# Performance work log

Hardware: AMD Instinct MI355X
Metric: run time of the kernel (lower is better)

Reference implementation:

```python
import jax, jax.numpy as jnp
import numpy as np


def setup_inputs() -> dict:
    key = jax.random.key(0)
    k1, k2 = jax.random.split(key)
    B, N, Fin, Fout, K = 4, 4096, 64, 64, 20
    x = jax.random.normal(k1, (B, N, Fin), dtype=jnp.float32)
    # nn.Linear(2*Fin, Fout): weight [Fout, 2*Fin], bias [Fout]
    W = jax.random.normal(k2, (Fout, 2 * Fin), dtype=jnp.float32) * (1.0 / np.sqrt(2 * Fin))
    b = jnp.zeros((Fout,), dtype=jnp.float32)
    return {"x": x, "W": W, "b": b, "k": K}


def _edge_features(x, k):
    # x: [B, N, F] -> edge features [B, N, k, 2F]
    # pairwise squared distance: ||xi||^2 - 2 xi.xj + ||xj||^2
    xs = jnp.sum(x * x, axis=2, keepdims=True)            # [B, N, 1]
    dist = xs - 2.0 * jnp.einsum('bnf,bmf->bnm', x, x) + jnp.swapaxes(xs, 1, 2)  # [B, N, N]
    idx = jnp.argsort(dist, axis=2)[:, :, 1:k + 1]        # skip self -> [B, N, k]
    # gather neighbor features per batch (vectorized index_select)
    neighbors = jax.vmap(lambda xb, ib: xb[ib])(x, idx)   # [B, N, k, F]
    central = jnp.broadcast_to(x[:, :, None, :], neighbors.shape)
    return jnp.concatenate([central, neighbors - central], axis=3)  # [B, N, k, 2F]


def reference(x, W, b, k):
    ee = _edge_features(x, k)                 # [B, N, k, 2F]
    h = jnp.einsum('bnkc,oc->bnko', ee, W) + b  # Linear(2F -> Fout)
    return jnp.max(h, axis=2)                 # max over k neighbors -> [B, N, Fout]
```

## Files before the change

### kernel.cpp

```cpp
#include <hip/hip_runtime.h>
#include <float.h>


constexpr int Bb = 4, Nn = 4096, Ff = 64, Kk = 20;

typedef __attribute__((ext_vector_type(8))) short bf16x8;
typedef __attribute__((ext_vector_type(16))) float f32x16;

__device__ inline unsigned int bf16rn(float f) {
  unsigned int u = __float_as_uint(f);
  return (u + 0x7fffu + ((u >> 16) & 1u)) >> 16;
}

constexpr int RT1 = 16;

__global__ __launch_bounds__(256) void uv_kernel2(
    const float* __restrict__ x, const float* __restrict__ W,
    const float* __restrict__ bvec, float* __restrict__ u,
    float* __restrict__ v, float* __restrict__ sq,
    unsigned short* __restrict__ xhi, unsigned short* __restrict__ xlo) {
  __shared__ __align__(16) float4 Ws[64 * 33];
  __shared__ __align__(16) float4 xs[RT1 * 16];
  const int t = threadIdx.x, l = t & 63, w = t >> 6;
  const int bn0 = blockIdx.x * RT1;
  #pragma unroll
  for (int i = 0; i < 8; i++) {
    int f = t + 256 * i;
    Ws[(f >> 5) * 33 + (f & 31)] = ((const float4*)W)[f];
  }
  xs[t] = ((const float4*)x)[bn0 * 16 + t];
  __syncthreads();
  #pragma unroll
  for (int i = 0; i < 4; i++) {
    int idx = t + 256 * i;
    int nloc = idx >> 6;
    int k = idx & 63;
    float val = ((const float*)xs)[idx];
    unsigned int hb = bf16rn(val);
    float fhi = __uint_as_float(hb << 16);
    unsigned int lb = bf16rn(val - fhi);
    int ng = bn0 + nloc;
    size_t flat = ((size_t)(ng >> 5) << 11) + ((size_t)(k >> 4) << 9) +
                  ((size_t)((k >> 3) & 1) << 8) + ((size_t)(ng & 31) << 3) +
                  (size_t)(k & 7);
    xhi[flat] = (unsigned short)hb;
    xlo[flat] = (unsigned short)lb;
  }
  #pragma unroll
  for (int i = 0; i < 4; i++) {
    int r = 4 * w + i;
    float val = ((const float*)&xs[r * 16])[l];
    float s = val * val;
    #pragma unroll
    for (int d = 32; d; d >>= 1) s += __shfl_xor(s, d, 64);
    if (l == 0) sq[bn0 + r] = s;
  }
  const int o = l;
  float ua[4] = {0.f, 0.f, 0.f, 0.f}, va[4] = {0.f, 0.f, 0.f, 0.f};
  #pragma unroll
  for (int c = 0; c < 16; c++) {
    float4 w1 = Ws[o * 33 + c];
    float4 w2 = Ws[o * 33 + 16 + c];
    float4 wd;
    wd.x = w1.x - w2.x; wd.y = w1.y - w2.y;
    wd.z = w1.z - w2.z; wd.w = w1.w - w2.w;
    #pragma unroll
    for (int i = 0; i < 4; i++) {
      float4 xv = xs[(4 * w + i) * 16 + c];
      ua[i] += xv.x * wd.x + xv.y * wd.y + xv.z * wd.z + xv.w * wd.w;
      va[i] += xv.x * w2.x + xv.y * w2.y + xv.z * w2.z + xv.w * w2.w;
    }
  }
  float bo = bvec[o];
  #pragma unroll
  for (int i = 0; i < 4; i++) {
    size_t row = (size_t)(bn0 + 4 * w + i);
    u[row * 64 + o] = ua[i] + bo;
    v[row * 64 + o] = va[i];
  }
}


__global__ __launch_bounds__(256) void key_mfma_kernel(
    const unsigned short* __restrict__ xhi,
    const unsigned short* __restrict__ xlo, const float* __restrict__ sq,
    unsigned short* __restrict__ keys) {
  const int t = threadIdx.x, l = t & 63, w = t >> 6;
  const int blk = blockIdx.x;
  const int b = blk >> 9;
  const int r = blk & 511;
  const int n_base = (r >> 2) * 32;
  const int m0w = (r & 3) * 1024 + w * 256;
  const int col = l & 31, half = l >> 5;

  const unsigned short* xhb = xhi + (size_t)b * Nn * Ff;
  const unsigned short* xlb = xlo + (size_t)b * Nn * Ff;
  const float* sqb = sq + b * Nn;

  bf16x8 Ahi[4], Alo[4];
  #pragma unroll
  for (int ks = 0; ks < 4; ks++) {
    size_t off = ((size_t)((n_base >> 5) * 4 + ks) << 9) + ((size_t)l << 3);
    Ahi[ks] = *(const bf16x8*)(xhb + off);
    Alo[ks] = *(const bf16x8*)(xlb + off);
  }
  float sqn_r[16];
  #pragma unroll
  for (int e = 0; e < 16; e++) {
    int row = (e & 3) + 8 * (e >> 2) + 4 * half;
    sqn_r[e] = sqb[n_base + row];
  }

  for (int j = 0; j < 8; ++j) {
    const int m0 = m0w + 32 * j;
    const int mblk = m0 >> 5;
    bf16x8 Bhi[4], Blo[4];
    #pragma unroll
    for (int ks = 0; ks < 4; ks++) {
      size_t off = ((size_t)(mblk * 4 + ks) << 9) + ((size_t)l << 3);
      Bhi[ks] = *(const bf16x8*)(xhb + off);
      Blo[ks] = *(const bf16x8*)(xlb + off);
    }
    f32x16 acc = {0.f, 0.f, 0.f, 0.f, 0.f, 0.f, 0.f, 0.f,
                  0.f, 0.f, 0.f, 0.f, 0.f, 0.f, 0.f, 0.f};
    #pragma unroll
    for (int ks = 0; ks < 4; ks++) {
      acc = __builtin_amdgcn_mfma_f32_32x32x16_bf16(Ahi[ks], Bhi[ks], acc, 0, 0, 0);
      acc = __builtin_amdgcn_mfma_f32_32x32x16_bf16(Ahi[ks], Blo[ks], acc, 0, 0, 0);
      acc = __builtin_amdgcn_mfma_f32_32x32x16_bf16(Alo[ks], Bhi[ks], acc, 0, 0, 0);
    }
    const int m = m0 + col;
    const float sm = sqb[m];
    #pragma unroll
    for (int e = 0; e < 16; e++) {
      int row = (e & 3) + 8 * (e >> 2) + 4 * half;
      int n = n_base + row;
      float d = fmaxf(sqn_r[e] + sm - 2.0f * acc[e], 0.f);
      unsigned int key = __float_as_uint(d) >> 15;
      if (m == n) key = 0xFFFFu;
      keys[((size_t)(b * Nn + n) << 12) + m] = (unsigned short)key;
    }
  }
}

__global__ __launch_bounds__(256) void select_kernel(
    const float* __restrict__ x, const unsigned short* __restrict__ keys,
    const float* __restrict__ u, const float* __restrict__ v,
    float* __restrict__ out) {
  __shared__ int candS[4 * 64];
  __shared__ unsigned long long keyS[4 * 64];
  __shared__ unsigned int histS[4][256];
  const int t = threadIdx.x, l = t & 63, w = t >> 6;
  const int row = blockIdx.x * 4 + w;
  const int rowu = __builtin_amdgcn_readfirstlane(row);
  const int b = rowu >> 12, n = rowu & (Nn - 1);
  const uint4* kr = (const uint4*)(keys + (size_t)rowu * Nn);
  uint4 kv[8];
  #pragma unroll
  for (int j = 0; j < 8; j++) kv[j] = kr[j * 64 + l];

  #pragma unroll
  for (int i = 0; i < 4; i++) histS[w][4 * l + i] = 0u;

  auto countLE = [&](int mid) -> int {
    int c = 0;
    #pragma unroll
    for (int j = 0; j < 8; j++) {
      unsigned int a0 = kv[j].x, a1 = kv[j].y, a2 = kv[j].z, a3 = kv[j].w;
      c += ((int)(a0 & 0xffffu) <= mid) + ((int)(a0 >> 16) <= mid);
      c += ((int)(a1 & 0xffffu) <= mid) + ((int)(a1 >> 16) <= mid);
      c += ((int)(a2 & 0xffffu) <= mid) + ((int)(a2 >> 16) <= mid);
      c += ((int)(a3 & 0xffffu) <= mid) + ((int)(a3 >> 16) <= mid);
    }
    #pragma unroll
    for (int d2 = 1; d2 < 64; d2 <<= 1) c += __shfl_xor(c, d2, 64);
    return c;
  };

  unsigned int mn = 0xffffffffu;
  #pragma unroll
  for (int j = 0; j < 8; j++) {
    unsigned int a0 = kv[j].x, a1 = kv[j].y, a2 = kv[j].z, a3 = kv[j].w;
    mn = min(mn, min(min(a0 & 0xffffu, a0 >> 16), min(a1 & 0xffffu, a1 >> 16)));
    mn = min(mn, min(min(a2 & 0xffffu, a2 >> 16), min(a3 & 0xffffu, a3 >> 16)));
  }
  #pragma unroll
  for (int d2 = 1; d2 < 64; d2 <<= 1)
    mn = min(mn, (unsigned int)__shfl_xor((int)mn, d2, 64));

  #pragma unroll
  for (int j = 0; j < 8; j++) {
    unsigned int a[4] = {kv[j].x, kv[j].y, kv[j].z, kv[j].w};
    #pragma unroll
    for (int e = 0; e < 4; e++) {
      unsigned int r0 = (a[e] & 0xffffu) - mn;
      unsigned int r1 = (a[e] >> 16) - mn;
      if (r0 < 256u) atomicAdd(&histS[w][r0], 1u);
      if (r1 < 256u) atomicAdd(&histS[w][r1], 1u);
    }
  }
  unsigned int s0 = histS[w][4 * l + 0], s1 = histS[w][4 * l + 1];
  unsigned int s2 = histS[w][4 * l + 2], s3 = histS[w][4 * l + 3];
  unsigned int ls = s0 + s1 + s2 + s3;
  unsigned int cum = ls;
  #pragma unroll
  for (int d2 = 1; d2 < 64; d2 <<= 1) {
    unsigned int o = (unsigned int)__shfl_up((int)cum, d2, 64);
    cum += (l >= d2) ? o : 0u;
  }
  unsigned int excl = cum - ls;
  unsigned int c0 = excl + s0, c1 = c0 + s1, c2 = c1 + s2;
  unsigned long long bal = __ballot(cum >= (unsigned int)Kk);

  int hc;
  if (bal != 0ull) {
    int b_loc = (c0 >= (unsigned)Kk) ? 0 : (c1 >= (unsigned)Kk) ? 1
              : (c2 >= (unsigned)Kk) ? 2 : 3;
    int flane = __ffsll((unsigned long long)bal) - 1;
    int hi_rel = __shfl(4 * l + b_loc, flane, 64);
    hc = (int)mn + hi_rel + 1;
  } else {
    int lo = (int)mn - 1;
    int hi = (int)mn + 64;
    if (hi > 65534) hi = 65534;
    int c = countLE(hi);
    int step = 128;
    while (c < Kk && hi < 65534) {
      lo = hi;
      hi += step;
      if (hi > 65534) hi = 65534;
      step <<= 1;
      c = countLE(hi);
    }
    while (c > 44 && hi - lo > 1) {
      int mid = (lo + hi) >> 1;
      int cm = countLE(mid);
      if (cm >= Kk) { hi = mid; c = cm; } else { lo = mid; }
    }
    hc = hi + 1;
  }

  int base = 0;
  #pragma unroll
  for (int j = 0; j < 8; j++) {
    unsigned int a[4] = {kv[j].x, kv[j].y, kv[j].z, kv[j].w};
    #pragma unroll
    for (int e = 0; e < 4; e++) {
      int pos = ((j * 64 + l) * 4 + e) * 2;
      {
        bool p = (int)(a[e] & 0xffffu) <= hc;
        unsigned long long m = __ballot(p);
        if (p) {
          int slot = base + __builtin_amdgcn_mbcnt_hi(
                                (unsigned int)(m >> 32),
                                __builtin_amdgcn_mbcnt_lo((unsigned int)m, 0));
          if (slot < 64) candS[w * 64 + slot] = pos;
        }
        base += __popcll(m);
      }
      {
        bool p = (int)(a[e] >> 16) <= hc;
        unsigned long long m = __ballot(p);
        if (p) {
          int slot = base + __builtin_amdgcn_mbcnt_hi(
                                (unsigned int)(m >> 32),
                                __builtin_amdgcn_mbcnt_lo((unsigned int)m, 0));
          if (slot < 64) candS[w * 64 + slot] = pos + 1;
        }
        base += __popcll(m);
      }
    }
  }
  int C = base;
  if (C > 64) C = 64;

  const float4* xb4 = (const float4*)(x + (size_t)b * Nn * Ff);
  unsigned long long key64 = 0xFFFFFFFF00000000ull | (unsigned int)l;
  if (l < C) {
    int mI = candS[w * 64 + l];
    const float4* xmf = xb4 + (size_t)mI * 16;
    float ds = 0.f;
    #pragma unroll
    for (int cc = 0; cc < 16; cc++) {
      float4 a = xb4[(size_t)n * 16 + cc];
      float4 bb = xmf[cc];
      float dx = a.x - bb.x, dy = a.y - bb.y, dz = a.z - bb.z, dw2 = a.w - bb.w;
      ds += dx * dx + dy * dy + dz * dz + dw2 * dw2;
    }
    if (mI == n) ds = FLT_MAX;
    key64 = ((unsigned long long)__float_as_uint(ds) << 32) | (unsigned int)mI;
  }

  keyS[w * 64 + l] = key64;
  const unsigned long long* kws = &keyS[w * 64];
  int rank = 0;
  #pragma unroll
  for (int j = 0; j < 64; j += 4) {
    rank += (kws[j] < key64) + (kws[j + 1] < key64) +
            (kws[j + 2] < key64) + (kws[j + 3] < key64);
  }
  if (rank < Kk)
    candS[w * 64 + rank] = (int)(key64 & 0xffffffffu) & (Nn - 1);

  const float* vb = v + (size_t)b * Nn * Ff;
  const size_t oidx = (size_t)rowu * 64 + l;
  float uo = u[oidx];
  float vv[Kk];
  #pragma unroll
  for (int i = 0; i < Kk; i++) {
    int mI = candS[w * 64 + i];
    vv[i] = vb[(size_t)mI * 64 + l];
  }
  float vmax = vv[0];
  #pragma unroll
  for (int i = 1; i < Kk; i++) vmax = fmaxf(vmax, vv[i]);
  out[oidx] = uo + vmax;
}

constexpr int RTF = 4;
constexpr int MTF = 64;
constexpr int TPADF = 17;
constexpr int CCAPF = 64;

__global__ __launch_bounds__(256) void knn_kernel(
    const float* __restrict__ x, const float* __restrict__ sq,
    const float* __restrict__ u, const float* __restrict__ v,
    float* __restrict__ out) {
  __shared__ __align__(16) float4 tileS[MTF * TPADF];
  __shared__ __align__(16) unsigned short keysS[RTF * Nn];
  __shared__ int candS[RTF * CCAPF];
  __shared__ int ccntS[RTF];
  const int t = threadIdx.x;
  const int l = t & 63, w = t >> 6;
  const int q = l & 15, g = l >> 4;
  const int bn0 = blockIdx.x * RTF;
  const int b = bn0 >> 12;
  const int n0 = bn0 & (Nn - 1);
  const float4* xb4 = (const float4*)(x + (size_t)b * Nn * Ff);
  const float* sqb = sq + b * Nn;
  if (t < RTF) ccntS[t] = 0;
  float4 xnq[RTF][4];
  #pragma unroll
  for (int r = 0; r < RTF; r++)
    #pragma unroll
    for (int c = 0; c < 4; c++) xnq[r][c] = xb4[(n0 + r) * 16 + 4 * g + c];
  const float sn = sqb[n0 + g];
  const int selfm = n0 + g;
  for (int T = 0; T < Nn / MTF; ++T) {
    __syncthreads();
    #pragma unroll
    for (int i = 0; i < 4; i++) {
      int f = t + 256 * i;
      tileS[(f >> 4) * TPADF + (f & 15)] = xb4[T * 1024 + f];
    }
    __syncthreads();
    const int mrow = 16 * w + q;
    const float4* xmp = &tileS[mrow * TPADF + 4 * g];
    float4 xm0 = xmp[0], xm1 = xmp[1], xm2 = xmp[2], xm3 = xmp[3];
    float dot[RTF];
    #pragma unroll
    for (int r = 0; r < RTF; r++) {
      float4 a0 = xnq[r][0], a1 = xnq[r][1], a2 = xnq[r][2], a3 = xnq[r][3];
      dot[r] = a0.x * xm0.x + a0.y * xm0.y + a0.z * xm0.z + a0.w * xm0.w +
               a1.x * xm1.x + a1.y * xm1.y + a1.z * xm1.z + a1.w * xm1.w +
               a2.x * xm2.x + a2.y * xm2.y + a2.z * xm2.z + a2.w * xm2.w +
               a3.x * xm3.x + a3.y * xm3.y + a3.z * xm3.z + a3.w * xm3.w;
    }
    #pragma unroll
    for (int r = 0; r < RTF; r++) {
      dot[r] += __shfl_xor(dot[r], 16, 64);
      dot[r] += __shfl_xor(dot[r], 32, 64);
    }
    float dg = (g == 0) ? dot[0] : (g == 1) ? dot[1] : (g == 2) ? dot[2] : dot[3];
    int m = T * MTF + mrow;
    float d = fmaxf(fmaf(-2.f, dg, sqb[m] + sn), 0.f);
    unsigned int key = __float_as_uint(d) >> 15;
    if (m == selfm) key = 0xFFFFu;
    keysS[g * Nn + m] = (unsigned short)key;
  }
  __syncthreads();
  const unsigned int* kp = (const unsigned int*)&keysS[w * Nn];
  int lo = -1, hi = 65535, cntHi = Nn;
  while (cntHi > 48 && hi - lo > 1) {
    int mid = (lo + hi) >> 1;
    unsigned int midu = (unsigned int)mid;
    int c = 0;
    #pragma unroll
    for (int cc = 0; cc < 8; ++cc) {
      int rc = (cc + l) & 7;
      uint4 k4 = *(const uint4*)(kp + l * 32 + rc * 4);
      c += ((k4.x & 0xffffu) <= midu) + ((k4.x >> 16) <= midu);
      c += ((k4.y & 0xffffu) <= midu) + ((k4.y >> 16) <= midu);
      c += ((k4.z & 0xffffu) <= midu) + ((k4.z >> 16) <= midu);
      c += ((k4.w & 0xffffu) <= midu) + ((k4.w >> 16) <= midu);
    }
    #pragma unroll
    for (int d2 = 1; d2 < 64; d2 <<= 1) c += __shfl_xor(c, d2, 64);
    if (c >= Kk) { hi = mid; cntHi = c; } else { lo = mid; }
  }
  {
    unsigned int hu = (unsigned int)hi;
    #pragma unroll
    for (int cc = 0; cc < 8; ++cc) {
      int rc = (cc + l) & 7;
      uint4 k4 = *(const uint4*)(kp + l * 32 + rc * 4);
      unsigned int ks[4] = {k4.x, k4.y, k4.z, k4.w};
      #pragma unroll
      for (int uu = 0; uu < 4; ++uu) {
        #pragma unroll
        for (int hh = 0; hh < 2; ++hh) {
          unsigned int kvv = hh ? (ks[uu] >> 16) : (ks[uu] & 0xffffu);
          if (kvv <= hu) {
            int slot = atomicAdd(&ccntS[w], 1);
            if (slot < CCAPF) candS[w * CCAPF + slot] = l * 64 + (rc * 4 + uu) * 2 + hh;
          }
        }
      }
    }
  }
  __syncthreads();
  const int n = n0 + w;
  const int C = min(cntHi, CCAPF);
  unsigned long long key64 = ~0ULL;
  if (l < C) {
    int mI = candS[w * CCAPF + l];
    const float4* xmf = xb4 + mI * 16;
    float ds = 0.f;
    #pragma unroll
    for (int c = 0; c < 16; c++) {
      float4 a = xb4[n * 16 + c];
      float4 bb = xmf[c];
      float dx = a.x - bb.x, dy = a.y - bb.y, dz = a.z - bb.z, dw2 = a.w - bb.w;
      ds += dx * dx + dy * dy + dz * dz + dw2 * dw2;
    }
    key64 = ((unsigned long long)__float_as_uint(ds) << 32) | (unsigned int)mI;
  }
  float vmax = -FLT_MAX;
  const float* vb = v + (size_t)b * Nn * Ff;
  #pragma unroll
  for (int it = 0; it < Kk; ++it) {
    unsigned long long kmin = key64;
    #pragma unroll
    for (int d2 = 1; d2 < 64; d2 <<= 1) {
      unsigned long long o =
          (unsigned long long)__shfl_xor((long long)kmin, d2, 64);
      kmin = (o < kmin) ? o : kmin;
    }
    int mI = (int)(kmin & 0xffffffffu) & (Nn - 1);
    vmax = fmaxf(vmax, vb[(size_t)mI * 64 + l]);
    if (key64 == kmin) key64 = ~0ULL;
  }
  const size_t oidx = (size_t)(bn0 + w) * 64 + l;
  out[oidx] = u[oidx] + vmax;
}

extern "C" void kernel_launch(void* const* d_in, const int* in_sizes, int n_in,
                              void* d_out, int out_size, void* d_ws,
                              size_t ws_size, hipStream_t stream) {
  const float* x = (const float*)d_in[0];
  const float* W = (const float*)d_in[1];
  const float* bvec = (const float*)d_in[2];
  float* u = (float*)d_ws;
  float* v = u + (size_t)Bb * Nn * Ff;
  float* sq = v + (size_t)Bb * Nn * Ff;
  unsigned short* xhi = (unsigned short*)(sq + (size_t)Bb * Nn);
  unsigned short* xlo = xhi + (size_t)Bb * Nn * Ff;
  unsigned short* keys = xlo + (size_t)Bb * Nn * Ff;
  float* out = (float*)d_out;
  const size_t need = (size_t)Bb * Nn * Ff * 4 * 2 + (size_t)Bb * Nn * 4 +
                      (size_t)Bb * Nn * Ff * 2 * 2 + (size_t)Bb * Nn * Nn * 2;

  uv_kernel2<<<Bb * Nn / RT1, 256, 0, stream>>>(x, W, bvec, u, v, sq, xhi, xlo);
  if (ws_size >= need) {
    key_mfma_kernel<<<Bb * Nn / 8, 256, 0, stream>>>(xhi, xlo, sq, keys);
    select_kernel<<<Bb * Nn / 4, 256, 0, stream>>>(x, keys, u, v, out);
  } else {
    knn_kernel<<<Bb * Nn / RTF, 256, 0, stream>>>(x, sq, u, v, out);
  }
}
```

Baseline: 148.8 us.

## Compress distance keys to 8-bit offsets from per-chunk minima

The key kernel now stages each 32x512 tile of 16-bit distance keys in shared memory and computes a per-row, per-512-column minimum. It writes that minimum as a 16-bit base plus 8-bit saturated offsets, which halves the dominant global key matrix traffic. The select kernel reconstructs keys as base plus byte for thresholding and histogramming. Candidate compaction now uses a per-lane count with a prefix scan instead of per-element ballots. Saturation at 255 can lose resolution, so more candidates may tie and overflow the 64-slot exact rerank.

```diff
diff --git a/kernel.cpp b/kernel.cpp
--- a/kernel.cpp
+++ b/kernel.cpp
@@ -81,17 +81,23 @@
 }
 
 
-__global__ __launch_bounds__(256) void key_mfma_kernel(
+__global__ __launch_bounds__(256) void key8_mfma_kernel(
     const unsigned short* __restrict__ xhi,
     const unsigned short* __restrict__ xlo, const float* __restrict__ sq,
-    unsigned short* __restrict__ keys) {
+    unsigned char* __restrict__ keys8, unsigned short* __restrict__ base16) {
+  __shared__ unsigned short keyL[32 * 520];
+  __shared__ unsigned int cminS[32];
   const int t = threadIdx.x, l = t & 63, w = t >> 6;
   const int blk = blockIdx.x;
-  const int b = blk >> 9;
-  const int r = blk & 511;
-  const int n_base = (r >> 2) * 32;
-  const int m0w = (r & 3) * 1024 + w * 256;
-  const int col = l & 31, half = l >> 5;
+  const int b = blk >> 10;
+  const int r = blk & 1023;
+  const int n_base = (r >> 3) * 32;
+  const int mchunk = r & 7;
+  const int chunk_base = mchunk * 512;
+  const int m0w = chunk_base + w * 128;
+  const int col = l & 31, hoff = (l >> 5) * 4;
+
+  if (t < 32) cminS[t] = 0xFFFFFFFFu;
 
   const unsigned short* xhb = xhi + (size_t)b * Nn * Ff;
   const unsigned short* xlb = xlo + (size_t)b * Nn * Ff;
@@ -106,12 +112,16 @@
   }
   float sqn_r[16];
   #pragma unroll
-  for (int e = 0; e < 16; e++) {
-    int row = (e & 3) + 8 * (e >> 2) + 4 * half;
-    sqn_r[e] = sqb[n_base + row];
-  }
-
-  for (int j = 0; j < 8; ++j) {
+  for (int e = 0; e < 16; e++)
+    sqn_r[e] = sqb[n_base + (e & 3) + 8 * (e >> 2) + hoff];
+  __syncthreads();
+
+  unsigned int kmin[16];
+  #pragma unroll
+  for (int e = 0; e < 16; e++) kmin[e] = 0xFFFFFFFFu;
+
+  #pragma unroll
+  for (int j = 0; j < 4; ++j) {
     const int m0 = m0w + 32 * j;
     const int mblk = m0 >> 5;
     bf16x8 Bhi[4], Blo[4];
@@ -130,77 +140,131 @@
       acc = __builtin_amdgcn_mfma_f32_32x32x16_bf16(Alo[ks], Bhi[ks], acc, 0, 0, 0);
     }
     const int m = m0 + col;
+    const int mloc = m - chunk_base;
     const float sm = sqb[m];
     #pragma unroll
     for (int e = 0; e < 16; e++) {
-      int row = (e & 3) + 8 * (e >> 2) + 4 * half;
-      int n = n_base + row;
+      int row = (e & 3) + 8 * (e >> 2) + hoff;
       float d = fmaxf(sqn_r[e] + sm - 2.0f * acc[e], 0.f);
       unsigned int key = __float_as_uint(d) >> 15;
-      if (m == n) key = 0xFFFFu;
-      keys[((size_t)(b * Nn + n) << 12) + m] = (unsigned short)key;
+      if (m == n_base + row) key = 0xFFFFu;
+      kmin[e] = min(kmin[e], key);
+      keyL[row * 520 + mloc] = (unsigned short)key;
+    }
+  }
+
+  #pragma unroll
+  for (int e = 0; e < 16; e++) {
+    unsigned int km = kmin[e];
+    #pragma unroll
+    for (int d2 = 1; d2 < 32; d2 <<= 1)
+      km = min(km, (unsigned int)__shfl_xor((int)km, d2, 64));
+    if (col == 0)
+      atomicMin(&cminS[(e & 3) + 8 * (e >> 2) + hoff], km);
+  }
+  __syncthreads();
+
+  if (t < 32)
+    base16[((size_t)(b * Nn + n_base + t) << 3) + mchunk] = (unsigned short)cminS[t];
+
+  {
+    const int prow = w * 8 + (l >> 3);
+    const unsigned int cb = cminS[prow];
+    const unsigned int* krow = (const unsigned int*)(keyL + prow * 520);
+    unsigned int* o32 = (unsigned int*)keys8 +
+                        ((size_t)(b * Nn + n_base + prow) << 10) + (mchunk << 7);
+    #pragma unroll
+    for (int i = 0; i < 16; i++) {
+      int oc = (l & 7) + 8 * i;
+      unsigned int lo = krow[2 * oc], hi = krow[2 * oc + 1];
+      unsigned int k0 = min((lo & 0xFFFFu) - cb, 255u);
+      unsigned int k1 = min((lo >> 16) - cb, 255u);
+      unsigned int k2 = min((hi & 0xFFFFu) - cb, 255u);
+      unsigned int k3 = min((hi >> 16) - cb, 255u);
+      o32[oc] = k0 | (k1 << 8) | (k2 << 16) | (k3 << 24);
     }
   }
 }
 
 __global__ __launch_bounds__(256) void select_kernel(
-    const float* __restrict__ x, const unsigned short* __restrict__ keys,
-    const float* __restrict__ u, const float* __restrict__ v,
-    float* __restrict__ out) {
-  __shared__ int candS[4 * 64];
-  __shared__ unsigned long long keyS[4 * 64];
-  __shared__ unsigned int histS[4][256];
+    const float* __restrict__ x, const unsigned char* __restrict__ keys8,
+    const unsigned short* __restrict__ base16, const float* __restrict__ u,
+    const float* __restrict__ v, float* __restrict__ out) {
+  __shared__ unsigned int histM[4][256];
+  __shared__ int candS[4][64];
+  __shared__ unsigned long long keyS[4][64];
   const int t = threadIdx.x, l = t & 63, w = t >> 6;
   const int row = blockIdx.x * 4 + w;
   const int rowu = __builtin_amdgcn_readfirstlane(row);
   const int b = rowu >> 12, n = rowu & (Nn - 1);
-  const uint4* kr = (const uint4*)(keys + (size_t)rowu * Nn);
-  uint4 kv[8];
-  #pragma unroll
-  for (int j = 0; j < 8; j++) kv[j] = kr[j * 64 + l];
-
-  #pragma unroll
-  for (int i = 0; i < 4; i++) histS[w][4 * l + i] = 0u;
+  const uint4* kr4 = (const uint4*)(keys8 + (size_t)rowu * Nn);
+  uint4 kv[4];
+  #pragma unroll
+  for (int j = 0; j < 4; j++) kv[j] = kr4[j * 64 + l];
+  unsigned int bs[4];
+  #pragma unroll
+  for (int j = 0; j < 4; j++)
+    bs[j] = base16[((size_t)rowu << 3) + 2 * j + (l >> 5)];
+
+  #pragma unroll
+  for (int i = 0; i < 4; i++) histM[w][4 * l + i] = 0u;
 
   auto countLE = [&](int mid) -> int {
     int c = 0;
     #pragma unroll
-    for (int j = 0; j < 8; j++) {
-      unsigned int a0 = kv[j].x, a1 = kv[j].y, a2 = kv[j].z, a3 = kv[j].w;
-      c += ((int)(a0 & 0xffffu) <= mid) + ((int)(a0 >> 16) <= mid);
-      c += ((int)(a1 & 0xffffu) <= mid) + ((int)(a1 >> 16) <= mid);
-      c += ((int)(a2 & 0xffffu) <= mid) + ((int)(a2 >> 16) <= mid);
-      c += ((int)(a3 & 0xffffu) <= mid) + ((int)(a3 >> 16) <= mid);
+    for (int j = 0; j < 4; j++) {
+      unsigned int a[4] = {kv[j].x, kv[j].y, kv[j].z, kv[j].w};
+      unsigned int bj = bs[j];
+      #pragma unroll
+      for (int q = 0; q < 4; q++) {
+        unsigned int xq = a[q];
+        c += ((int)(bj + (xq & 255u)) <= mid) +
+             ((int)(bj + ((xq >> 8) & 255u)) <= mid) +
+             ((int)(bj + ((xq >> 16) & 255u)) <= mid) +
+             ((int)(bj + (xq >> 24)) <= mid);
+      }
     }
     #pragma unroll
     for (int d2 = 1; d2 < 64; d2 <<= 1) c += __shfl_xor(c, d2, 64);
     return c;
   };
 
-  unsigned int mn = 0xffffffffu;
-  #pragma unroll
-  for (int j = 0; j < 8; j++) {
-    unsigned int a0 = kv[j].x, a1 = kv[j].y, a2 = kv[j].z, a3 = kv[j].w;
-    mn = min(mn, min(min(a0 & 0xffffu, a0 >> 16), min(a1 & 0xffffu, a1 >> 16)));
-    mn = min(mn, min(min(a2 & 0xffffu, a2 >> 16), min(a3 & 0xffffu, a3 >> 16)));
+  unsigned int mn = 0xFFFFFFFFu;
+  #pragma unroll
+  for (int j = 0; j < 4; j++) {
+    unsigned int a[4] = {kv[j].x, kv[j].y, kv[j].z, kv[j].w};
+    unsigned int bm = 255u;
+    #pragma unroll
+    for (int q = 0; q < 4; q++) {
+      unsigned int xq = a[q];
+      bm = min(bm, min(min(xq & 255u, (xq >> 8) & 255u),
+                       min((xq >> 16) & 255u, xq >> 24)));
+    }
+    mn = min(mn, bs[j] + bm);
   }
   #pragma unroll
   for (int d2 = 1; d2 < 64; d2 <<= 1)
     mn = min(mn, (unsigned int)__shfl_xor((int)mn, d2, 64));
 
   #pragma unroll
-  for (int j = 0; j < 8; j++) {
+  for (int j = 0; j < 4; j++) {
     unsigned int a[4] = {kv[j].x, kv[j].y, kv[j].z, kv[j].w};
-    #pragma unroll
-    for (int e = 0; e < 4; e++) {
-      unsigned int r0 = (a[e] & 0xffffu) - mn;
-      unsigned int r1 = (a[e] >> 16) - mn;
-      if (r0 < 256u) atomicAdd(&histS[w][r0], 1u);
-      if (r1 < 256u) atomicAdd(&histS[w][r1], 1u);
-    }
-  }
-  unsigned int s0 = histS[w][4 * l + 0], s1 = histS[w][4 * l + 1];
-  unsigned int s2 = histS[w][4 * l + 2], s3 = histS[w][4 * l + 3];
+    unsigned int bj = bs[j];
+    #pragma unroll
+    for (int q = 0; q < 4; q++) {
+      unsigned int xq = a[q];
+      unsigned int r0 = bj + (xq & 255u) - mn;
+      unsigned int r1 = bj + ((xq >> 8) & 255u) - mn;
+      unsigned int r2 = bj + ((xq >> 16) & 255u) - mn;
+      unsigned int r3 = bj + (xq >> 24) - mn;
+      if (r0 < 256u) atomicAdd(&histM[w][r0], 1u);
+      if (r1 < 256u) atomicAdd(&histM[w][r1], 1u);
+      if (r2 < 256u) atomicAdd(&histM[w][r2], 1u);
+      if (r3 < 256u) atomicAdd(&histM[w][r3], 1u);
+    }
+  }
+  unsigned int s0 = histM[w][4 * l + 0], s1 = histM[w][4 * l + 1];
+  unsigned int s2 = histM[w][4 * l + 2], s3 = histM[w][4 * l + 3];
   unsigned int ls = s0 + s1 + s2 + s3;
   unsigned int cum = ls;
   #pragma unroll
@@ -216,19 +280,19 @@
   if (bal != 0ull) {
     int b_loc = (c0 >= (unsigned)Kk) ? 0 : (c1 >= (unsigned)Kk) ? 1
               : (c2 >= (unsigned)Kk) ? 2 : 3;
-    int flane = __ffsll((unsigned long long)bal) - 1;
+    int flane = __ffsll(bal) - 1;
     int hi_rel = __shfl(4 * l + b_loc, flane, 64);
     hc = (int)mn + hi_rel + 1;
   } else {
     int lo = (int)mn - 1;
     int hi = (int)mn + 64;
-    if (hi > 65534) hi = 65534;
+    if (hi > 66046) hi = 66046;
     int c = countLE(hi);
     int step = 128;
-    while (c < Kk && hi < 65534) {
+    while (c < Kk && hi < 66046) {
       lo = hi;
       hi += step;
-      if (hi > 65534) hi = 65534;
+      if (hi > 66046) hi = 66046;
       step <<= 1;
       c = countLE(hi);
     }
@@ -240,44 +304,52 @@
     hc = hi + 1;
   }
 
-  int base = 0;
-  #pragma unroll
-  for (int j = 0; j < 8; j++) {
+  int myc = 0;
+  #pragma unroll
+  for (int j = 0; j < 4; j++) {
     unsigned int a[4] = {kv[j].x, kv[j].y, kv[j].z, kv[j].w};
-    #pragma unroll
-    for (int e = 0; e < 4; e++) {
-      int pos = ((j * 64 + l) * 4 + e) * 2;
-      {
-        bool p = (int)(a[e] & 0xffffu) <= hc;
-        unsigned long long m = __ballot(p);
-        if (p) {
-          int slot = base + __builtin_amdgcn_mbcnt_hi(
-                                (unsigned int)(m >> 32),
-                                __builtin_amdgcn_mbcnt_lo((unsigned int)m, 0));
-          if (slot < 64) candS[w * 64 + slot] = pos;
+    unsigned int bj = bs[j];
+    #pragma unroll
+    for (int q = 0; q < 4; q++) {
+      unsigned int xq = a[q];
+      myc += ((int)(bj + (xq & 255u)) <= hc) +
+             ((int)(bj + ((xq >> 8) & 255u)) <= hc) +
+             ((int)(bj + ((xq >> 16) & 255u)) <= hc) +
+             ((int)(bj + (xq >> 24)) <= hc);
+    }
+  }
+  int incl = myc;
+  #pragma unroll
+  for (int d2 = 1; d2 < 64; d2 <<= 1) {
+    int o = __shfl_up(incl, d2, 64);
+    incl += (l >= d2) ? o : 0;
+  }
+  int C = __shfl(incl, 63);
+  int off = incl - myc;
+  #pragma unroll
+  for (int j = 0; j < 4; j++) {
+    unsigned int a[4] = {kv[j].x, kv[j].y, kv[j].z, kv[j].w};
+    unsigned int bj = bs[j];
+    #pragma unroll
+    for (int q = 0; q < 4; q++) {
+      unsigned int xq = a[q];
+      int mbase = ((j * 64 + l) * 4 + q) * 4;
+      #pragma unroll
+      for (int i = 0; i < 4; i++) {
+        unsigned int byte = (xq >> (8 * i)) & 255u;
+        if ((int)(bj + byte) <= hc) {
+          if (off < 64) candS[w][off] = mbase + i;
+          off++;
         }
-        base += __popcll(m);
       }
-      {
-        bool p = (int)(a[e] >> 16) <= hc;
-        unsigned long long m = __ballot(p);
-        if (p) {
-          int slot = base + __builtin_amdgcn_mbcnt_hi(
-                                (unsigned int)(m >> 32),
-                                __builtin_amdgcn_mbcnt_lo((unsigned int)m, 0));
-          if (slot < 64) candS[w * 64 + slot] = pos + 1;
-        }
-        base += __popcll(m);
-      }
-    }
-  }
-  int C = base;
+    }
+  }
   if (C > 64) C = 64;
 
   const float4* xb4 = (const float4*)(x + (size_t)b * Nn * Ff);
   unsigned long long key64 = 0xFFFFFFFF00000000ull | (unsigned int)l;
   if (l < C) {
-    int mI = candS[w * 64 + l];
+    int mI = candS[w][l];
     const float4* xmf = xb4 + (size_t)mI * 16;
     float ds = 0.f;
     #pragma unroll
@@ -291,16 +363,15 @@
     key64 = ((unsigned long long)__float_as_uint(ds) << 32) | (unsigned int)mI;
   }
 
-  keyS[w * 64 + l] = key64;
-  const unsigned long long* kws = &keyS[w * 64];
+  keyS[w][l] = key64;
   int rank = 0;
   #pragma unroll
-  for (int j = 0; j < 64; j += 4) {
-    rank += (kws[j] < key64) + (kws[j + 1] < key64) +
-            (kws[j + 2] < key64) + (kws[j + 3] < key64);
+  for (int q = 0; q < 64; q += 4) {
+    rank += (keyS[w][q] < key64) + (keyS[w][q + 1] < key64) +
+            (keyS[w][q + 2] < key64) + (keyS[w][q + 3] < key64);
   }
   if (rank < Kk)
-    candS[w * 64 + rank] = (int)(key64 & 0xffffffffu) & (Nn - 1);
+    candS[w][rank] = (int)(key64 & 0xffffffffu) & (Nn - 1);
 
   const float* vb = v + (size_t)b * Nn * Ff;
   const size_t oidx = (size_t)rowu * 64 + l;
@@ -308,7 +379,7 @@
   float vv[Kk];
   #pragma unroll
   for (int i = 0; i < Kk; i++) {
-    int mI = candS[w * 64 + i];
+    int mI = candS[w][i];
     vv[i] = vb[(size_t)mI * 64 + l];
   }
   float vmax = vv[0];
@@ -465,15 +536,18 @@
   float* sq = v + (size_t)Bb * Nn * Ff;
   unsigned short* xhi = (unsigned short*)(sq + (size_t)Bb * Nn);
   unsigned short* xlo = xhi + (size_t)Bb * Nn * Ff;
-  unsigned short* keys = xlo + (size_t)Bb * Nn * Ff;
+  unsigned short* base16 = xlo + (size_t)Bb * Nn * Ff;
+  unsigned char* keys8 = (unsigned char*)(base16 + (size_t)Bb * Nn * 8);
   float* out = (float*)d_out;
   const size_t need = (size_t)Bb * Nn * Ff * 4 * 2 + (size_t)Bb * Nn * 4 +
-                      (size_t)Bb * Nn * Ff * 2 * 2 + (size_t)Bb * Nn * Nn * 2;
+                      (size_t)Bb * Nn * Ff * 2 * 2 +
+                      (size_t)Bb * Nn * 8 * 2 +
+                      (size_t)Bb * Nn * Nn;
 
   uv_kernel2<<<Bb * Nn / RT1, 256, 0, stream>>>(x, W, bvec, u, v, sq, xhi, xlo);
   if (ws_size >= need) {
-    key_mfma_kernel<<<Bb * Nn / 8, 256, 0, stream>>>(xhi, xlo, sq, keys);
-    select_kernel<<<Bb * Nn / 4, 256, 0, stream>>>(x, keys, u, v, out);
+    key8_mfma_kernel<<<Bb * Nn / 4, 256, 0, stream>>>(xhi, xlo, sq, keys8, base16);
+    select_kernel<<<Bb * Nn / 4, 256, 0, stream>>>(x, keys8, base16, u, v, out);
   } else {
     knn_kernel<<<Bb * Nn / RTF, 256, 0, stream>>>(x, sq, u, v, out);
   }
```

After: 213.7 us. +43.6%, slower.
